# Optimization experiments

Measured on AMD Instinct MI355X. Metric: run time of the kernel, lower is better.

The kernel has to match this reference:

```python
import jax, jax.numpy as jnp
import numpy as np

HIDDEN = 32
DN = ('NCHW', 'OIHW', 'NCHW')


def setup_inputs() -> dict:
    key = jax.random.key(0)
    ks = jax.random.split(key, 16)
    B = 32768
    s = lambda *sh: 1.0 / np.sqrt(np.prod(sh[1:]) if len(sh) > 1 else sh[0])
    inp = {
        'x': jax.random.normal(ks[0], (B, 12, 3, 4, 4), jnp.float32),
        'hour': jax.random.uniform(ks[1], (B, 1), jnp.float32),
        # ConvLSTM cell: Conv2d(3+32 -> 4*32, k=3, pad=1)
        'conv_w': jax.random.normal(ks[2], (4 * HIDDEN, 3 + HIDDEN, 3, 3), jnp.float32) * 0.05,
        'conv_b': jnp.zeros((4 * HIDDEN,), jnp.float32),
        # hour embedding: Linear(1,16) -> ReLU -> Linear(16,32)
        'he_w1': jax.random.normal(ks[3], (1, 16), jnp.float32),
        'he_b1': jnp.zeros((16,), jnp.float32),
        'he_w2': jax.random.normal(ks[4], (16, 32), jnp.float32) * 0.25,
        'he_b2': jnp.zeros((32,), jnp.float32),
        # decoder: Linear(544,256) -> ReLU -> Linear(256,128) -> ReLU -> Linear(128,30) -> Sigmoid
        'd_w1': jax.random.normal(ks[5], (32 * 4 * 4 + 32, 256), jnp.float32) * 0.04,
        'd_b1': jnp.zeros((256,), jnp.float32),
        'd_w2': jax.random.normal(ks[6], (256, 128), jnp.float32) * 0.06,
        'd_b2': jnp.zeros((128,), jnp.float32),
        'd_w3': jax.random.normal(ks[7], (128, 30), jnp.float32) * 0.09,
        'd_b3': jnp.zeros((30,), jnp.float32),
    }
    return inp


def _convlstm_scan(x, conv_w, conv_b):
    B, T, C, H, W = x.shape
    h0 = jnp.zeros((B, HIDDEN, H, W), x.dtype)
    c0 = jnp.zeros((B, HIDDEN, H, W), x.dtype)

    def step(carry, xt):
        h, c = carry
        inp = jnp.concatenate([xt, h], axis=1)  # [B, 3+32, 4, 4]
        gates = jax.lax.conv_general_dilated(
            inp, conv_w, (1, 1), 'SAME', dimension_numbers=DN)
        gates = gates + conv_b[None, :, None, None]
        i, f, o, g = jnp.split(gates, 4, axis=1)
        c_next = jax.nn.sigmoid(f) * c + jax.nn.sigmoid(i) * jnp.tanh(g)
        h_next = jax.nn.sigmoid(o) * jnp.tanh(c_next)
        return (h_next, c_next), None

    xs = jnp.swapaxes(x, 0, 1)  # [T, B, C, H, W]
    (h, c), _ = jax.lax.scan(step, (h0, c0), xs)
    return h


def reference(x, hour, conv_w, conv_b, he_w1, he_b1, he_w2, he_b2,
              d_w1, d_b1, d_w2, d_b2, d_w3, d_b3):
    B = x.shape[0]
    h = _convlstm_scan(x, conv_w, conv_b)            # [B, 32, 4, 4]
    spatial = h.reshape(B, -1)                        # [B, 512]
    hf = jax.nn.relu(hour @ he_w1 + he_b1) @ he_w2 + he_b2  # [B, 32]
    z = jnp.concatenate([spatial, hf], axis=1)        # [B, 544]
    z = jax.nn.relu(z @ d_w1 + d_b1)
    z = jax.nn.relu(z @ d_w2 + d_b2)                  # (dropout is identity in eval)
    out = jax.nn.sigmoid(z @ d_w3 + d_b3)
    return out.reshape(B, 10, 3)
```

## Files before the change

### kernel.cpp

```cpp
#include <hip/hip_runtime.h>

typedef _Float16 f16;
typedef _Float16 f16x4 __attribute__((ext_vector_type(4)));
typedef _Float16 f16x8 __attribute__((ext_vector_type(8)));
typedef float f32x2 __attribute__((ext_vector_type(2)));
typedef float f32x4 __attribute__((ext_vector_type(4)));

#define MFMA16(a, b, c) __builtin_amdgcn_mfma_f32_16x16x32_f16((a), (b), (c), 0, 0, 0)

__device__ __forceinline__ float rcp_(float x) { return __builtin_amdgcn_rcpf(x); }
__device__ __forceinline__ float sigm(float v) { return rcp_(1.0f + __expf(-v)); }
__device__ __forceinline__ float tanh_(float v) { return 1.0f - 2.0f * rcp_(__expf(2.0f * v) + 1.0f); }
__device__ __forceinline__ float exp2_(float x) { return __builtin_amdgcn_exp2f(x); }

#define LOG2E 1.4426950408889634f
#define HCELL 80
#define HSAMP 2880
#define HBUFB 11520
#define XP0 23040
#define XBUFB 1152
#define WSO 25344
#define SMEMA 43776
#define NGRP 8192
#define GRID_REC 512

extern "C" __global__ __launch_bounds__(256, 2)
void hwq_rec(const float* __restrict__ gx, const float* __restrict__ ghour,
             const float* __restrict__ gcw, const float* __restrict__ gcb,
             const float* __restrict__ ghw1, const float* __restrict__ ghb1,
             const float* __restrict__ ghw2, const float* __restrict__ ghb2,
             f16* __restrict__ wz)
{
  __shared__ __align__(16) char smem[SMEMA];
  const int tid = threadIdx.x;
  const int lane = tid & 63;
  const int wv = tid >> 6;
  const int mg = wv & 1;
  const int ng = wv >> 1;
  const int lr = lane & 15;
  const int lk = lane >> 4;
  const int TOFF[9] = {0, 1, 2, 6, 7, 8, 12, 13, 14};
  const int pp0 = (lr >> 2) * 6 + (lr & 3);

  {
    float* za = (float*)smem;
    for (int i = tid; i < 6336; i += 256) za[i] = 0.0f;
    f16* axs = (f16*)(smem + WSO);
    for (int i = tid; i < 4096; i += 256) {
      int m = i >> 5, k = i & 31;
      int tau = k >> 2, sl = k & 3;
      int oc = ((m & 3) << 5) + (m >> 2);
      float sc = ((m & 3) == 3) ? (2.0f * LOG2E) : (-LOG2E);
      f16 v = (f16)0.0f;
      if (sl < 3) v = (f16)(sc * gcw[oc * 315 + sl * 9 + tau]);
      else if (tau == 4) v = (f16)(sc * gcb[oc]);
      axs[i] = v;
    }
    __syncthreads();
  }
  f16x8 Ax1[4], Ax2[4];
  {
    if (tid < 128) {
      int xb = tid >> 6, b = (tid >> 4) & 3, p = tid & 15;
      int cell = ((p >> 2) + 1) * 6 + (p & 3) + 1;
      *(f16*)(smem + XP0 + xb * XBUFB + b * 288 + cell * 8 + 6) = (f16)1.0f;
    }
    #pragma unroll
    for (int mt = 0; mt < 4; ++mt) {
      Ax1[mt] = *(const f16x8*)(smem + WSO + (mg * 64 + mt * 16 + lr) * 64 + lk * 16);
      int m = mg * 64 + mt * 16 + lr;
      int oc = ((m & 3) << 5) + (m >> 2);
      float sc = ((m & 3) == 3) ? (2.0f * LOG2E) : (-LOG2E);
      f16x8 f = {(f16)0, (f16)0, (f16)0, (f16)0, (f16)0, (f16)0, (f16)0, (f16)0};
      if (lk == 0) {
        f[0] = (f16)(sc * gcw[oc * 315 + 8]);
        f[1] = (f16)(sc * gcw[oc * 315 + 17]);
        f[2] = (f16)(sc * gcw[oc * 315 + 26]);
      }
      Ax2[mt] = f;
    }
    __syncthreads();
  }
  f16x8 Ah[9][4];
  {
    f16* wst = (f16*)(smem + WSO);
    #pragma unroll
    for (int c = 0; c < 4; ++c) {
      for (int i = tid; i < 9216; i += 256) {
        int mrow = i / 288, rem = i - mrow * 288;
        int m = c * 32 + mrow;
        int oc = ((m & 3) << 5) + (m >> 2);
        float sc = ((m & 3) == 3) ? (2.0f * LOG2E) : (-LOG2E);
        wst[i] = (f16)(sc * gcw[oc * 315 + 27 + rem]);
      }
      __syncthreads();
      if (mg == (c >> 1)) {
        #pragma unroll
        for (int mtl = 0; mtl < 2; ++mtl) {
          int mt = (c & 1) * 2 + mtl;
          #pragma unroll
          for (int tap = 0; tap < 9; ++tap) {
            f16x8 f;
            #pragma unroll
            for (int j = 0; j < 8; ++j)
              f[j] = wst[(mtl * 16 + lr) * 288 + (lk * 8 + j) * 9 + tap];
            Ah[tap][mt] = f;
          }
        }
      }
      __syncthreads();
    }
  }

  const int hb  = (ng * 2) * HSAMP + pp0 * HCELL + lk * 16;
  const int xpb = XP0 + (ng * 2) * 288 + pp0 * 8;
  const int wb  = (ng * 2) * HSAMP + (pp0 + 7) * HCELL + (mg * 16 + lk) * 2;
  const int xo0 = TOFF[2 * lk] * 8;
  const int xo1 = TOFF[2 * lk + 1] * 8;
  const bool stg = tid < 192;
  const int sb = tid / 48, srem = tid - sb * 48;
  const int sp = srem & 15, sic = srem >> 4;
  const int xdst = XP0 + sb * 288 + (((sp >> 2) + 1) * 6 + (sp & 3) + 1) * 8 + sic * 2;
  const int zb_ = tid >> 6, zc16 = (tid >> 2) & 15, zpart = tid & 3;
  const int zaddr = zb_ * HSAMP + ((zc16 >> 2) * 6 + (zc16 & 3) + 7) * HCELL + zpart * 16;

  const f32x4 Z0v = {0.f, 0.f, 0.f, 0.f};

#define XPH(nt) { \
    const int base_ = xrb + xpb + (nt) * 288; \
    f16x4 lo_ = *(const f16x4*)(smem + base_ + xo0); \
    f16x4 hi_ = *(const f16x4*)(smem + base_ + xo1); \
    f16x8 bf1_ = __builtin_shufflevector(lo_, hi_, 0, 1, 2, 3, 4, 5, 6, 7); \
    f16x4 l8_ = *(const f16x4*)(smem + base_ + 112); \
    f16x8 bf2_ = __builtin_shufflevector(l8_, l8_, 0, 1, 2, 3, 0, 1, 2, 3); \
    _Pragma("unroll") for (int mt = 0; mt < 4; ++mt) { \
      acc[mt][nt] = MFMA16(Ax1[mt], bf1_, Z0v); \
      acc[mt][nt] = MFMA16(Ax2[mt], bf2_, acc[mt][nt]); } }

#define TAPS(nt, t0, t1) \
    _Pragma("unroll") for (int tap = (t0); tap < (t1); ++tap) { \
      f16x8 bf_ = *(const f16x8*)(smem + rb + hb + TOFF[tap] * HCELL + (nt) * HSAMP); \
      _Pragma("unroll") for (int mt = 0; mt < 4; ++mt) \
        acc[mt][nt] = MFMA16(Ah[tap][mt], bf_, acc[mt][nt]); }

#define UPD_L(mt, nt) { \
    float Ei = exp2_(acc[mt][nt][0]); \
    float Ef = exp2_(acc[mt][nt][1]); \
    float Eo = exp2_(acc[mt][nt][2]); \
    float Eg = exp2_(acc[mt][nt][3]); \
    float fg = rcp_(1.0f + Ef); \
    float pq = rcp_((1.0f + Ei) * (1.0f + Eg)); \
    float cn = fmaf(fg, cst[mt][nt], (2.0f * LOG2E) * ((Eg - 1.0f) * pq)); \
    cst[mt][nt] = cn; \
    float Ec = exp2_(cn); \
    *(f16*)(smem + wbuf + wb + (nt) * HSAMP + (mt) * 8) = \
        (f16)((Ec - 1.0f) * rcp_((1.0f + Eo) * (1.0f + Ec))); }

#define UPD_G(mt, nt) { \
    float Ei = exp2_(acc[mt][nt][0]); \
    float Ef = exp2_(acc[mt][nt][1]); \
    float Eo = exp2_(acc[mt][nt][2]); \
    float Eg = exp2_(acc[mt][nt][3]); \
    float fg = rcp_(1.0f + Ef); \
    float pq = rcp_((1.0f + Ei) * (1.0f + Eg)); \
    float cn = fmaf(fg, cst[mt][nt], (2.0f * LOG2E) * ((Eg - 1.0f) * pq)); \
    float Ec = exp2_(cn); \
    wz[(size_t)(bg + ng * 2 + (nt)) * 544 + (mg * 16 + (mt) * 4 + lk) * 16 + lr] = \
        (f16)((Ec - 1.0f) * rcp_((1.0f + Eo) * (1.0f + Ec))); }

  for (int grp = blockIdx.x; grp < NGRP; grp += GRID_REC) {
    const int bg = grp << 2;
    const float* gxb = gx + (size_t)bg * 576;
    const float* xsrc = gxb + (size_t)sb * 576 + srem;

    {
      f32x2 z2 = {0.f, 0.f};
      *(f32x2*)(smem + zaddr) = z2;
      *(f32x2*)(smem + zaddr + 8) = z2;
    }
    if (stg) *(f16*)(smem + xdst) = (f16)xsrc[0];
    float cst[4][2];
    #pragma unroll
    for (int mt = 0; mt < 4; ++mt) { cst[mt][0] = 0.0f; cst[mt][1] = 0.0f; }
    __syncthreads();

    for (int t = 0; t < 11; ++t) {
      const int rb   = (t & 1) * HBUFB;
      const int xrb  = (t & 1) * XBUFB;
      const int wbuf = HBUFB - rb;
      float xv = 0.0f;
      if (stg) xv = xsrc[(t + 1) * 48];

      f32x4 acc[4][2];
      XPH(0); TAPS(0, 0, 9);
      XPH(1); TAPS(1, 0, 4);
      UPD_L(0, 0); UPD_L(1, 0); UPD_L(2, 0); UPD_L(3, 0);
      TAPS(1, 4, 9);
      UPD_L(0, 1); UPD_L(1, 1); UPD_L(2, 1); UPD_L(3, 1);

      if (stg) *(f16*)(smem + (XBUFB - xrb) + xdst) = (f16)xv;
      __syncthreads();
    }

    {
      const int rb  = HBUFB;
      const int xrb = XBUFB;
      f32x4 acc[4][2];
      XPH(0); TAPS(0, 0, 9);
      XPH(1); TAPS(1, 0, 4);
      UPD_G(0, 0); UPD_G(1, 0); UPD_G(2, 0); UPD_G(3, 0);
      TAPS(1, 4, 9);
      UPD_G(0, 1); UPD_G(1, 1); UPD_G(2, 1); UPD_G(3, 1);

      if (tid < 128) {
        int b = tid >> 5, k2 = tid & 31;
        float h0 = ghour[bg + b];
        float a = ghb2[k2];
        #pragma unroll
        for (int ii = 0; ii < 16; ++ii) {
          float u = fmaxf(h0 * ghw1[ii] + ghb1[ii], 0.0f);
          a += u * ghw2[ii * 32 + k2];
        }
        wz[(size_t)(bg + b) * 544 + 512 + k2] = (f16)a;
      }
    }
  }
#undef XPH
#undef TAPS
#undef UPD_L
#undef UPD_G
}

extern "C" __global__ void hwq_prep(const float* __restrict__ gdw1,
                                    const float* __restrict__ gdw2,
                                    const float* __restrict__ gdw3,
                                    f16* __restrict__ w1t, f16* __restrict__ w2t,
                                    f16* __restrict__ w3t)
{
  int i0 = blockIdx.x * 256 + threadIdx.x;
  int stride = gridDim.x * 256;
  for (int idx = i0; idx < 139264; idx += stride) {
    int n = idx / 544, k = idx - n * 544;
    w1t[idx] = (f16)gdw1[k * 256 + n];
  }
  for (int idx = i0; idx < 32768; idx += stride) {
    int n = idx >> 8, k = idx & 255;
    w2t[idx] = (f16)gdw2[k * 128 + n];
  }
  for (int idx = i0; idx < 4096; idx += stride) {
    int n = idx >> 7, k = idx & 127;
    w3t[idx] = (n < 30) ? (f16)gdw3[k * 30 + n] : (f16)0.0f;
  }
}

extern "C" __global__ __launch_bounds__(256, 2)
void hwq_dec(const f16* __restrict__ wz, const f16* __restrict__ w1t,
             const f16* __restrict__ w2t, const f16* __restrict__ w3t,
             const float* __restrict__ gdb1, const float* __restrict__ gdb2,
             const float* __restrict__ gdb3, float* __restrict__ gout)
{
  __shared__ __align__(16) char smem[55296];
  f16* a1 = (f16*)smem;
  f16* a2 = (f16*)(smem + 35840);
  const int tid = threadIdx.x;
  const int lane = tid & 63;
  const int wv = tid >> 6;
  const int lr = lane & 15;
  const int lk = lane >> 4;
  const int s0 = blockIdx.x << 6;

  f32x4 acc1[4][4];
  #pragma unroll
  for (int nt = 0; nt < 4; ++nt) {
    float bb = gdb1[wv * 64 + nt * 16 + lr];
    f32x4 bv = {bb, bb, bb, bb};
    #pragma unroll
    for (int mt = 0; mt < 4; ++mt) acc1[mt][nt] = bv;
  }
  for (int kt = 0; kt < 17; ++kt) {
    f16x8 af[4];
    #pragma unroll
    for (int mt = 0; mt < 4; ++mt)
      af[mt] = *(const f16x8*)(wz + (size_t)(s0 + mt * 16 + lr) * 544 + kt * 32 + lk * 8);
    #pragma unroll
    for (int nt = 0; nt < 4; ++nt) {
      f16x8 bf = *(const f16x8*)(w1t + (size_t)(wv * 64 + nt * 16 + lr) * 544 + kt * 32 + lk * 8);
      #pragma unroll
      for (int mt = 0; mt < 4; ++mt)
        acc1[mt][nt] = MFMA16(af[mt], bf, acc1[mt][nt]);
    }
  }
  #pragma unroll
  for (int mt = 0; mt < 4; ++mt)
    #pragma unroll
    for (int nt = 0; nt < 4; ++nt) {
      int n = wv * 64 + nt * 16 + lr;
      #pragma unroll
      for (int r = 0; r < 4; ++r)
        a1[(mt * 16 + lk * 4 + r) * 280 + n] = (f16)fmaxf(acc1[mt][nt][r], 0.0f);
    }
  __syncthreads();

  f32x4 acc2[4][2];
  #pragma unroll
  for (int nt = 0; nt < 2; ++nt) {
    float bb = gdb2[wv * 32 + nt * 16 + lr];
    f32x4 bv = {bb, bb, bb, bb};
    #pragma unroll
    for (int mt = 0; mt < 4; ++mt) acc2[mt][nt] = bv;
  }
  for (int kt = 0; kt < 8; ++kt) {
    f16x8 af[4];
    #pragma unroll
    for (int mt = 0; mt < 4; ++mt)
      af[mt] = *(const f16x8*)(a1 + (mt * 16 + lr) * 280 + kt * 32 + lk * 8);
    #pragma unroll
    for (int nt = 0; nt < 2; ++nt) {
      f16x8 bf = *(const f16x8*)(w2t + (size_t)(wv * 32 + nt * 16 + lr) * 256 + kt * 32 + lk * 8);
      #pragma unroll
      for (int mt = 0; mt < 4; ++mt)
        acc2[mt][nt] = MFMA16(af[mt], bf, acc2[mt][nt]);
    }
  }
  __syncthreads();
  #pragma unroll
  for (int mt = 0; mt < 4; ++mt)
    #pragma unroll
    for (int nt = 0; nt < 2; ++nt) {
      int n = wv * 32 + nt * 16 + lr;
      #pragma unroll
      for (int r = 0; r < 4; ++r)
        a2[(mt * 16 + lk * 4 + r) * 152 + n] = (f16)fmaxf(acc2[mt][nt][r], 0.0f);
    }
  __syncthreads();

  if (wv < 2) {
    int n = wv * 16 + lr;
    float bb = (n < 30) ? gdb3[n] : 0.0f;
    f32x4 acc3[4];
    #pragma unroll
    for (int mt = 0; mt < 4; ++mt) { f32x4 bv = {bb, bb, bb, bb}; acc3[mt] = bv; }
    #pragma unroll
    for (int kt = 0; kt < 4; ++kt) {
      f16x8 bf = *(const f16x8*)(w3t + n * 128 + kt * 32 + lk * 8);
      #pragma unroll
      for (int mt = 0; mt < 4; ++mt) {
        f16x8 af = *(const f16x8*)(a2 + (mt * 16 + lr) * 152 + kt * 32 + lk * 8);
        acc3[mt] = MFMA16(af, bf, acc3[mt]);
      }
    }
    if (n < 30) {
      #pragma unroll
      for (int mt = 0; mt < 4; ++mt)
        #pragma unroll
        for (int r = 0; r < 4; ++r)
          gout[(size_t)(s0 + mt * 16 + lk * 4 + r) * 30 + n] = sigm(acc3[mt][r]);
    }
  }
}

typedef _Float16 f16x4m __attribute__((ext_vector_type(4)));
#define OFF_B 46080
#define SMEM_BYTES (46080 + 17408)

extern "C" __global__ __launch_bounds__(256, 1)
void hwq_fused_mono(const float* __restrict__ gx, const float* __restrict__ ghour,
               const float* __restrict__ gcw, const float* __restrict__ gcb,
               const float* __restrict__ ghw1, const float* __restrict__ ghb1,
               const float* __restrict__ ghw2, const float* __restrict__ ghb2,
               const float* __restrict__ gdw1, const float* __restrict__ gdb1,
               const float* __restrict__ gdw2, const float* __restrict__ gdb2,
               const float* __restrict__ gdw3, const float* __restrict__ gdb3,
               float* __restrict__ gout)
{
  __shared__ __align__(16) char smem[SMEM_BYTES];
  const int tid = threadIdx.x;
  const int lane = tid & 63;
  const int wv = tid >> 6;
  const int mg = wv & 1;
  const int ng = wv >> 1;
  const int lr = lane & 15;
  const int lk = lane >> 4;
  const int bg = blockIdx.x << 4;

  f16x8 Ah[9][4];
  {
    f16* wst = (f16*)(smem);
    #pragma unroll
    for (int c = 0; c < 2; ++c) {
      __syncthreads();
      for (int i = tid; i < 18432; i += 256) {
        int oc = i / 288, rem = i - oc * 288;
        wst[i] = (f16)gcw[(c * 64 + oc) * 315 + 27 + rem];
      }
      __syncthreads();
      #pragma unroll
      for (int g = 0; g < 2; ++g) {
        int ocl = g * 32 + mg * 16 + lr;
        #pragma unroll
        for (int tap = 0; tap < 9; ++tap) {
          f16x8 f;
          #pragma unroll
          for (int j = 0; j < 8; ++j)
            f[j] = wst[ocl * 288 + (lk * 8 + j) * 9 + tap];
          Ah[tap][c * 2 + g] = f;
        }
      }
    }
  }
  f16x8 Ax[4];
  {
    f16* xw = (f16*)(smem + OFF_B);
    __syncthreads();
    for (int i = tid; i < 3456; i += 256) {
      int oc = i / 27, rem = i - oc * 27;
      xw[i] = (f16)gcw[oc * 315 + rem];
    }
    __syncthreads();
    #pragma unroll
    for (int mt = 0; mt < 4; ++mt) {
      int oc = mt * 32 + mg * 16 + lr;
      f16x8 f;
      #pragma unroll
      for (int j = 0; j < 8; ++j) {
        int k = lk * 8 + j;
        int tap = (k * 11) >> 5;
        int ic = k - 3 * tap;
        f16 v = (f16)0.0f;
        if (k < 27) v = xw[oc * 27 + ic * 9 + tap];
        f[j] = v;
      }
      Ax[mt] = f;
    }
    __syncthreads();
  }

  float bias[4][4];
  #pragma unroll
  for (int mt = 0; mt < 4; ++mt)
    #pragma unroll
    for (int r = 0; r < 4; ++r)
      bias[mt][r] = gcb[mt * 32 + mg * 16 + lk * 4 + r];

  {
    float* za = (float*)smem;
    for (int i = tid; i < 11520; i += 256) za[i] = 0.0f;
    float* zb = (float*)(smem + OFF_B);
    for (int i = tid; i < 1152; i += 256) zb[i] = 0.0f;
    __syncthreads();
    for (int i = tid; i < 768; i += 256) {
      int b = i / 48, rem = i - b * 48;
      int pos = rem & 15;
      int ic = rem >> 4;
      int pp = (pos >> 2) * 6 + (pos & 3) + 7;
      *(f16*)(smem + OFF_B + b * 288 + pp * 8 + ic * 2) =
          (f16)gx[(size_t)(bg + b) * 576 + rem];
    }
    __syncthreads();
  }

  int hbase[8], xbase[8], wbase[8];
  #pragma unroll
  for (int nt = 0; nt < 8; ++nt) {
    int n = ng * 128 + nt * 16 + lr;
    int b = n >> 4, pos = n & 15;
    int pp0 = (pos >> 2) * 6 + (pos & 3);
    hbase[nt] = b * 2880 + pp0 * 80 + lk * 16;
    xbase[nt] = OFF_B + b * 288 + pp0 * 8;
    wbase[nt] = b * 2880 + (pp0 + 7) * 80 + (mg * 16 + lk * 4) * 2;
  }
  int xoff[8], xval[8];
  #pragma unroll
  for (int j = 0; j < 8; ++j) {
    int k = lk * 8 + j;
    int tap = (k * 11) >> 5;
    int ic = k - 3 * tap;
    xoff[j] = ((tap / 3) * 6 + (tap % 3)) * 8 + ic * 2;
    xval[j] = (k < 27);
  }

  const int TOFF[9] = {0, 1, 2, 6, 7, 8, 12, 13, 14};

  f32x4 cst[8];
  #pragma unroll
  for (int nt = 0; nt < 8; ++nt) { f32x4 z = {0.f, 0.f, 0.f, 0.f}; cst[nt] = z; }

  for (int t = 0; t < 12; ++t) {
    f32x4 acc[4][8];
    #pragma unroll
    for (int mt = 0; mt < 4; ++mt) {
      f32x4 bi = {bias[mt][0], bias[mt][1], bias[mt][2], bias[mt][3]};
      #pragma unroll
      for (int nt = 0; nt < 8; ++nt) acc[mt][nt] = bi;
    }
    #pragma unroll
    for (int tap = 0; tap < 9; ++tap) {
      #pragma unroll
      for (int nt = 0; nt < 8; ++nt) {
        f16x8 bf = *(const f16x8*)(smem + hbase[nt] + TOFF[tap] * 80);
        #pragma unroll
        for (int mt = 0; mt < 4; ++mt)
          acc[mt][nt] = MFMA16(Ah[tap][mt], bf, acc[mt][nt]);
      }
    }
    #pragma unroll
    for (int nt = 0; nt < 8; ++nt) {
      f16x8 bf;
      #pragma unroll
      for (int j = 0; j < 8; ++j) {
        int a = xval[j] ? (xbase[nt] + xoff[j]) : OFF_B;
        bf[j] = *(const f16*)(smem + a);
      }
      #pragma unroll
      for (int mt = 0; mt < 4; ++mt)
        acc[mt][nt] = MFMA16(Ax[mt], bf, acc[mt][nt]);
    }
    __syncthreads();

    #pragma unroll
    for (int nt = 0; nt < 8; ++nt) {
      f16 hh[4];
      #pragma unroll
      for (int r = 0; r < 4; ++r) {
        float ig = sigm(acc[0][nt][r]);
        float fg = sigm(acc[1][nt][r]);
        float og = sigm(acc[2][nt][r]);
        float gg = tanh_(acc[3][nt][r]);
        float cn = fg * cst[nt][r] + ig * gg;
        cst[nt][r] = cn;
        hh[r] = (f16)(og * tanh_(cn));
      }
      if (t < 11) {
        f16x4m hv = {hh[0], hh[1], hh[2], hh[3]};
        *(f16x4m*)(smem + wbase[nt]) = hv;
      } else {
        int n = ng * 128 + nt * 16 + lr;
        int b = n >> 4, pos = n & 15;
        int ch0 = mg * 16 + lk * 4;
        #pragma unroll
        for (int r = 0; r < 4; ++r)
          *(f16*)(smem + OFF_B + b * 1088 + (ch0 + r) * 32 + pos * 2) = hh[r];
      }
    }
    if (t < 11) {
      for (int i = tid; i < 768; i += 256) {
        int b = i / 48, rem = i - b * 48;
        int pos = rem & 15;
        int ic = rem >> 4;
        int pp = (pos >> 2) * 6 + (pos & 3) + 7;
        *(f16*)(smem + OFF_B + b * 288 + pp * 8 + ic * 2) =
            (f16)gx[(size_t)(bg + b) * 576 + (t + 1) * 48 + rem];
      }
    } else {
      for (int i = tid; i < 512; i += 256) {
        int b = i >> 5, k2 = i & 31;
        float h0 = ghour[bg + b];
        float a = ghb2[k2];
        #pragma unroll
        for (int ii = 0; ii < 16; ++ii) {
          float u = fmaxf(h0 * ghw1[ii] + ghb1[ii], 0.0f);
          a += u * ghw2[ii * 32 + k2];
        }
        *(f16*)(smem + OFF_B + b * 1088 + (512 + k2) * 2) = (f16)a;
      }
    }
    __syncthreads();
  }

  f16* zz  = (f16*)(smem + OFF_B);
  f16* wch = (f16*)(smem);
  f16* a1  = (f16*)(smem + 16384);
  f16* a2  = (f16*)(smem + 24576);
  f16* w3s = (f16*)(smem + 28672);

  f32x4 acc1[4];
  #pragma unroll
  for (int i = 0; i < 4; ++i) { f32x4 z = {0.f, 0.f, 0.f, 0.f}; acc1[i] = z; }
  for (int kt = 0; kt < 17; ++kt) {
    __syncthreads();
    for (int i = tid; i < 8192; i += 256) {
      int k = i >> 8, n = i & 255;
      wch[i] = (f16)gdw1[(kt * 32 + k) * 256 + n];
    }
    __syncthreads();
    f16x8 af = *(const f16x8*)((char*)zz + lr * 1088 + (kt * 32 + lk * 8) * 2);
    #pragma unroll
    for (int nt = 0; nt < 4; ++nt) {
      int n = (wv * 4 + nt) * 16 + lr;
      f16x8 bf;
      #pragma unroll
      for (int j = 0; j < 8; ++j) bf[j] = wch[(lk * 8 + j) * 256 + n];
      acc1[nt] = MFMA16(af, bf, acc1[nt]);
    }
  }
  __syncthreads();
  #pragma unroll
  for (int nt = 0; nt < 4; ++nt) {
    int n = (wv * 4 + nt) * 16 + lr;
    float bb = gdb1[n];
    #pragma unroll
    for (int r = 0; r < 4; ++r)
      a1[(lk * 4 + r) * 256 + n] = (f16)fmaxf(acc1[nt][r] + bb, 0.0f);
  }

  f32x4 acc2[2];
  #pragma unroll
  for (int i = 0; i < 2; ++i) { f32x4 z = {0.f, 0.f, 0.f, 0.f}; acc2[i] = z; }
  for (int kt = 0; kt < 8; ++kt) {
    __syncthreads();
    for (int i = tid; i < 4096; i += 256) {
      int k = i >> 7, n = i & 127;
      wch[i] = (f16)gdw2[(kt * 32 + k) * 128 + n];
    }
    __syncthreads();
    f16x8 af = *(const f16x8*)((char*)a1 + lr * 512 + (kt * 32 + lk * 8) * 2);
    #pragma unroll
    for (int nt = 0; nt < 2; ++nt) {
      int n = (wv * 2 + nt) * 16 + lr;
      f16x8 bf;
      #pragma unroll
      for (int j = 0; j < 8; ++j) bf[j] = wch[(lk * 8 + j) * 128 + n];
      acc2[nt] = MFMA16(af, bf, acc2[nt]);
    }
  }
  __syncthreads();
  #pragma unroll
  for (int nt = 0; nt < 2; ++nt) {
    int n = (wv * 2 + nt) * 16 + lr;
    float bb = gdb2[n];
    #pragma unroll
    for (int r = 0; r < 4; ++r)
      a2[(lk * 4 + r) * 128 + n] = (f16)fmaxf(acc2[nt][r] + bb, 0.0f);
  }
  __syncthreads();

  for (int i = tid; i < 4096; i += 256) {
    int k = i >> 5, n = i & 31;
    w3s[i] = (n < 30) ? (f16)gdw3[k * 30 + n] : (f16)0.0f;
  }
  __syncthreads();
  if (wv < 2) {
    f32x4 acc3 = {0.f, 0.f, 0.f, 0.f};
    int n = wv * 16 + lr;
    #pragma unroll
    for (int kt = 0; kt < 4; ++kt) {
      f16x8 af = *(const f16x8*)((char*)a2 + lr * 256 + (kt * 32 + lk * 8) * 2);
      f16x8 bf;
      #pragma unroll
      for (int j = 0; j < 8; ++j) bf[j] = w3s[(kt * 32 + lk * 8 + j) * 32 + n];
      acc3 = MFMA16(af, bf, acc3);
    }
    if (n < 30) {
      float bb = gdb3[n];
      #pragma unroll
      for (int r = 0; r < 4; ++r) {
        float v = sigm(acc3[r] + bb);
        gout[(size_t)(bg + lk * 4 + r) * 30 + n] = v;
      }
    }
  }
}

extern "C" void kernel_launch(void* const* d_in, const int* in_sizes, int n_in,
                              void* d_out, int out_size, void* d_ws, size_t ws_size,
                              hipStream_t stream) {
  (void)in_sizes; (void)n_in; (void)out_size;
  const size_t W1OFF = 35651584;
  const size_t W2OFF = W1OFF + 278528;
  const size_t W3OFF = W2OFF + 65536;
  const size_t NEED  = W3OFF + 8192;
  if (ws_size >= NEED) {
    f16* wzp = (f16*)d_ws;
    f16* w1t = (f16*)((char*)d_ws + W1OFF);
    f16* w2t = (f16*)((char*)d_ws + W2OFF);
    f16* w3t = (f16*)((char*)d_ws + W3OFF);
    hwq_prep<<<256, 256, 0, stream>>>((const float*)d_in[8], (const float*)d_in[10],
                                      (const float*)d_in[12], w1t, w2t, w3t);
    hwq_rec<<<GRID_REC, 256, 0, stream>>>(
        (const float*)d_in[0], (const float*)d_in[1], (const float*)d_in[2],
        (const float*)d_in[3], (const float*)d_in[4], (const float*)d_in[5],
        (const float*)d_in[6], (const float*)d_in[7], wzp);
    hwq_dec<<<512, 256, 0, stream>>>(wzp, w1t, w2t, w3t,
                                     (const float*)d_in[9], (const float*)d_in[11],
                                     (const float*)d_in[13], (float*)d_out);
  } else {
    hwq_fused_mono<<<2048, 256, 0, stream>>>(
        (const float*)d_in[0],  (const float*)d_in[1],  (const float*)d_in[2],
        (const float*)d_in[3],  (const float*)d_in[4],  (const float*)d_in[5],
        (const float*)d_in[6],  (const float*)d_in[7],  (const float*)d_in[8],
        (const float*)d_in[9],  (const float*)d_in[10], (const float*)d_in[11],
        (const float*)d_in[12], (const float*)d_in[13], (float*)d_out);
  }
}
```

Before: 676.0 us.

## Interleave two independent sample groups per block in ConvLSTM recurrence

Each block now runs the ConvLSTM recurrence for two sample groups at once, using a second shared-memory region for hidden state and inputs and separate cell-state registers. The MFMA and gate-update work of the two groups is interleaved, so one group's dependent latency can be hidden by the other's work within the serial time loop. This costs more LDS per block and more live registers, which may limit occupancy or cause spills.

```diff
diff --git a/kernel.cpp b/kernel.cpp
--- a/kernel.cpp
+++ b/kernel.cpp
@@ -19,8 +19,9 @@
 #define HBUFB 11520
 #define XP0 23040
 #define XBUFB 1152
+#define AR 25344
 #define WSO 25344
-#define SMEMA 43776
+#define SMEMA 50688
 #define NGRP 8192
 #define GRID_REC 512
 
@@ -42,9 +43,8 @@
   const int TOFF[9] = {0, 1, 2, 6, 7, 8, 12, 13, 14};
   const int pp0 = (lr >> 2) * 6 + (lr & 3);
 
+  f16x8 Ax1[4], Ax2[4];
   {
-    float* za = (float*)smem;
-    for (int i = tid; i < 6336; i += 256) za[i] = 0.0f;
     f16* axs = (f16*)(smem + WSO);
     for (int i = tid; i < 4096; i += 256) {
       int m = i >> 5, k = i & 31;
@@ -57,14 +57,6 @@
       axs[i] = v;
     }
     __syncthreads();
-  }
-  f16x8 Ax1[4], Ax2[4];
-  {
-    if (tid < 128) {
-      int xb = tid >> 6, b = (tid >> 4) & 3, p = tid & 15;
-      int cell = ((p >> 2) + 1) * 6 + (p & 3) + 1;
-      *(f16*)(smem + XP0 + xb * XBUFB + b * 288 + cell * 8 + 6) = (f16)1.0f;
-    }
     #pragma unroll
     for (int mt = 0; mt < 4; ++mt) {
       Ax1[mt] = *(const f16x8*)(smem + WSO + (mg * 64 + mt * 16 + lr) * 64 + lk * 16);
@@ -111,6 +103,17 @@
       __syncthreads();
     }
   }
+  {
+    float* za = (float*)smem;
+    for (int i = tid; i < 12672; i += 256) za[i] = 0.0f;
+    __syncthreads();
+    {
+      int ar = tid >> 7, xb = (tid >> 6) & 1, b = (tid >> 4) & 3, p = tid & 15;
+      int cell = ((p >> 2) + 1) * 6 + (p & 3) + 1;
+      *(f16*)(smem + ar * AR + XP0 + xb * XBUFB + b * 288 + cell * 8 + 6) = (f16)1.0f;
+    }
+    __syncthreads();
+  }
 
   const int hb  = (ng * 2) * HSAMP + pp0 * HCELL + lk * 16;
   const int xpb = XP0 + (ng * 2) * 288 + pp0 * 8;
@@ -126,8 +129,8 @@
 
   const f32x4 Z0v = {0.f, 0.f, 0.f, 0.f};
 
-#define XPH(nt) { \
-    const int base_ = xrb + xpb + (nt) * 288; \
+#define XPH(ab, nt) { \
+    const int base_ = (ab) + xrb + xpb + (nt) * 288; \
     f16x4 lo_ = *(const f16x4*)(smem + base_ + xo0); \
     f16x4 hi_ = *(const f16x4*)(smem + base_ + xo1); \
     f16x8 bf1_ = __builtin_shufflevector(lo_, hi_, 0, 1, 2, 3, 4, 5, 6, 7); \
@@ -137,68 +140,83 @@
       acc[mt][nt] = MFMA16(Ax1[mt], bf1_, Z0v); \
       acc[mt][nt] = MFMA16(Ax2[mt], bf2_, acc[mt][nt]); } }
 
-#define TAPS(nt, t0, t1) \
-    _Pragma("unroll") for (int tap = (t0); tap < (t1); ++tap) { \
-      f16x8 bf_ = *(const f16x8*)(smem + rb + hb + TOFF[tap] * HCELL + (nt) * HSAMP); \
+#define TAPS(ab, nt) \
+    _Pragma("unroll") for (int tap = 0; tap < 9; ++tap) { \
+      f16x8 bf_ = *(const f16x8*)(smem + (ab) + rb + hb + TOFF[tap] * HCELL + (nt) * HSAMP); \
       _Pragma("unroll") for (int mt = 0; mt < 4; ++mt) \
         acc[mt][nt] = MFMA16(Ah[tap][mt], bf_, acc[mt][nt]); }
 
-#define UPD_L(mt, nt) { \
+#define UPD_L(g, ab, mt, nt) { \
     float Ei = exp2_(acc[mt][nt][0]); \
     float Ef = exp2_(acc[mt][nt][1]); \
     float Eo = exp2_(acc[mt][nt][2]); \
     float Eg = exp2_(acc[mt][nt][3]); \
     float fg = rcp_(1.0f + Ef); \
     float pq = rcp_((1.0f + Ei) * (1.0f + Eg)); \
-    float cn = fmaf(fg, cst[mt][nt], (2.0f * LOG2E) * ((Eg - 1.0f) * pq)); \
-    cst[mt][nt] = cn; \
+    float cn = fmaf(fg, cst[g][mt][nt], (2.0f * LOG2E) * ((Eg - 1.0f) * pq)); \
+    cst[g][mt][nt] = cn; \
     float Ec = exp2_(cn); \
-    *(f16*)(smem + wbuf + wb + (nt) * HSAMP + (mt) * 8) = \
+    *(f16*)(smem + (ab) + wbuf + wb + (nt) * HSAMP + (mt) * 8) = \
         (f16)((Ec - 1.0f) * rcp_((1.0f + Eo) * (1.0f + Ec))); }
 
-#define UPD_G(mt, nt) { \
+#define UPD_G(g, bgv, mt, nt) { \
     float Ei = exp2_(acc[mt][nt][0]); \
     float Ef = exp2_(acc[mt][nt][1]); \
     float Eo = exp2_(acc[mt][nt][2]); \
     float Eg = exp2_(acc[mt][nt][3]); \
     float fg = rcp_(1.0f + Ef); \
     float pq = rcp_((1.0f + Ei) * (1.0f + Eg)); \
-    float cn = fmaf(fg, cst[mt][nt], (2.0f * LOG2E) * ((Eg - 1.0f) * pq)); \
+    float cn = fmaf(fg, cst[g][mt][nt], (2.0f * LOG2E) * ((Eg - 1.0f) * pq)); \
     float Ec = exp2_(cn); \
-    wz[(size_t)(bg + ng * 2 + (nt)) * 544 + (mg * 16 + (mt) * 4 + lk) * 16 + lr] = \
+    wz[(size_t)((bgv) + ng * 2 + (nt)) * 544 + (mg * 16 + (mt) * 4 + lk) * 16 + lr] = \
         (f16)((Ec - 1.0f) * rcp_((1.0f + Eo) * (1.0f + Ec))); }
 
-  for (int grp = blockIdx.x; grp < NGRP; grp += GRID_REC) {
-    const int bg = grp << 2;
-    const float* gxb = gx + (size_t)bg * 576;
-    const float* xsrc = gxb + (size_t)sb * 576 + srem;
+  for (int it = 0; it < 8; ++it) {
+    const int gA = blockIdx.x + (2 * it) * GRID_REC;
+    const int gB = gA + GRID_REC;
+    const int bgA = gA << 2, bgB = gB << 2;
+    const float* xsrcA = gx + (size_t)bgA * 576 + (size_t)sb * 576 + srem;
+    const float* xsrcB = gx + (size_t)bgB * 576 + (size_t)sb * 576 + srem;
 
     {
       f32x2 z2 = {0.f, 0.f};
       *(f32x2*)(smem + zaddr) = z2;
       *(f32x2*)(smem + zaddr + 8) = z2;
-    }
-    if (stg) *(f16*)(smem + xdst) = (f16)xsrc[0];
-    float cst[4][2];
-    #pragma unroll
-    for (int mt = 0; mt < 4; ++mt) { cst[mt][0] = 0.0f; cst[mt][1] = 0.0f; }
+      *(f32x2*)(smem + AR + zaddr) = z2;
+      *(f32x2*)(smem + AR + zaddr + 8) = z2;
+    }
+    if (stg) {
+      *(f16*)(smem + xdst) = (f16)xsrcA[0];
+      *(f16*)(smem + AR + xdst) = (f16)xsrcB[0];
+    }
+    float cst[2][4][2];
+    #pragma unroll
+    for (int g = 0; g < 2; ++g)
+      #pragma unroll
+      for (int mt = 0; mt < 4; ++mt) { cst[g][mt][0] = 0.0f; cst[g][mt][1] = 0.0f; }
     __syncthreads();
 
     for (int t = 0; t < 11; ++t) {
       const int rb   = (t & 1) * HBUFB;
       const int xrb  = (t & 1) * XBUFB;
       const int wbuf = HBUFB - rb;
-      float xv = 0.0f;
-      if (stg) xv = xsrc[(t + 1) * 48];
+      float xvA = 0.0f, xvB = 0.0f;
+      if (stg) { xvA = xsrcA[(t + 1) * 48]; xvB = xsrcB[(t + 1) * 48]; }
 
       f32x4 acc[4][2];
-      XPH(0); TAPS(0, 0, 9);
-      XPH(1); TAPS(1, 0, 4);
-      UPD_L(0, 0); UPD_L(1, 0); UPD_L(2, 0); UPD_L(3, 0);
-      TAPS(1, 4, 9);
-      UPD_L(0, 1); UPD_L(1, 1); UPD_L(2, 1); UPD_L(3, 1);
-
-      if (stg) *(f16*)(smem + (XBUFB - xrb) + xdst) = (f16)xv;
+      XPH(0, 0); TAPS(0, 0);
+      XPH(0, 1); TAPS(0, 1);
+      UPD_L(0, 0, 0, 0); UPD_L(0, 0, 1, 0); UPD_L(0, 0, 2, 0); UPD_L(0, 0, 3, 0);
+      XPH(AR, 0); TAPS(AR, 0);
+      UPD_L(0, 0, 0, 1); UPD_L(0, 0, 1, 1); UPD_L(0, 0, 2, 1); UPD_L(0, 0, 3, 1);
+      XPH(AR, 1); TAPS(AR, 1);
+      UPD_L(1, AR, 0, 0); UPD_L(1, AR, 1, 0); UPD_L(1, AR, 2, 0); UPD_L(1, AR, 3, 0);
+      UPD_L(1, AR, 0, 1); UPD_L(1, AR, 1, 1); UPD_L(1, AR, 2, 1); UPD_L(1, AR, 3, 1);
+
+      if (stg) {
+        *(f16*)(smem + (XBUFB - xrb) + xdst) = (f16)xvA;
+        *(f16*)(smem + AR + (XBUFB - xrb) + xdst) = (f16)xvB;
+      }
       __syncthreads();
     }
 
@@ -206,22 +224,26 @@
       const int rb  = HBUFB;
       const int xrb = XBUFB;
       f32x4 acc[4][2];
-      XPH(0); TAPS(0, 0, 9);
-      XPH(1); TAPS(1, 0, 4);
-      UPD_G(0, 0); UPD_G(1, 0); UPD_G(2, 0); UPD_G(3, 0);
-      TAPS(1, 4, 9);
-      UPD_G(0, 1); UPD_G(1, 1); UPD_G(2, 1); UPD_G(3, 1);
-
-      if (tid < 128) {
+      XPH(0, 0); TAPS(0, 0);
+      XPH(0, 1); TAPS(0, 1);
+      UPD_G(0, bgA, 0, 0); UPD_G(0, bgA, 1, 0); UPD_G(0, bgA, 2, 0); UPD_G(0, bgA, 3, 0);
+      XPH(AR, 0); TAPS(AR, 0);
+      UPD_G(0, bgA, 0, 1); UPD_G(0, bgA, 1, 1); UPD_G(0, bgA, 2, 1); UPD_G(0, bgA, 3, 1);
+      XPH(AR, 1); TAPS(AR, 1);
+      UPD_G(1, bgB, 0, 0); UPD_G(1, bgB, 1, 0); UPD_G(1, bgB, 2, 0); UPD_G(1, bgB, 3, 0);
+      UPD_G(1, bgB, 0, 1); UPD_G(1, bgB, 1, 1); UPD_G(1, bgB, 2, 1); UPD_G(1, bgB, 3, 1);
+
+      {
         int b = tid >> 5, k2 = tid & 31;
-        float h0 = ghour[bg + b];
+        int smp = (b < 4) ? (bgA + b) : (bgB + b - 4);
+        float h0 = ghour[smp];
         float a = ghb2[k2];
         #pragma unroll
         for (int ii = 0; ii < 16; ++ii) {
           float u = fmaxf(h0 * ghw1[ii] + ghb1[ii], 0.0f);
           a += u * ghw2[ii * 32 + k2];
         }
-        wz[(size_t)(bg + b) * 544 + 512 + k2] = (f16)a;
+        wz[(size_t)smp * 544 + 512 + k2] = (f16)a;
       }
     }
   }
```

New measurement: 643.3 us. 1.05x faster.
